# Kernel tuning notes

Hardware: AMD Instinct MI355X
Metric: run time of the kernel (lower is better)

The kernel has to match this reference:

```python
import jax, jax.numpy as jnp
import numpy as np

N_HEAD = 16
ROPE_BASE = 10000.0


def setup_inputs() -> dict:
    key = jax.random.key(0)
    k1, k2, k3 = jax.random.split(key, 3)
    B, T, C = 2, 2048, 2048
    x = jax.random.normal(k1, (B, T, C), dtype=jnp.float32)
    # 0.02 init scale keeps attention logits in a sane range
    w_qkv = jax.random.normal(k2, (3 * C, C), dtype=jnp.float32) * 0.02
    w_proj = jax.random.normal(k3, (C, C), dtype=jnp.float32) * 0.02
    return {"x": x, "w_qkv": w_qkv, "w_proj": w_proj}


def _apply_rope(t, cos, sin):
    # t: [B, T, H, hd]; cos/sin: [T, hd//2]
    B, T, H, hd = t.shape
    ts = t.reshape(B, T, H, hd // 2, 2)
    x0, x1 = ts[..., 0], ts[..., 1]
    c = cos[None, :, None, :]
    s = sin[None, :, None, :]
    out = jnp.stack([x0 * c - x1 * s, x1 * c + x0 * s], axis=-1)
    return out.reshape(B, T, H, hd)


def reference(x, w_qkv, w_proj):
    B, T, C = x.shape
    H = N_HEAD
    hd = C // H

    qkv = x @ w_qkv.T                       # [B, T, 3C]
    q, k, v = jnp.split(qkv, 3, axis=2)
    q = q.reshape(B, T, H, hd)
    k = k.reshape(B, T, H, hd)              # present kv: pre-RoPE k, [B,T,H,hd]
    v = v.reshape(B, T, H, hd).transpose(0, 2, 1, 3)  # [B,H,T,hd]

    # RoPE cache (positions = arange(T) since past_key_value is None)
    theta = 1.0 / (ROPE_BASE ** (jnp.arange(0, hd, 2, dtype=jnp.float32) / hd))
    ang = jnp.arange(T, dtype=jnp.float32)[:, None] * theta[None, :]  # [T, hd//2]
    cos, sin = jnp.cos(ang), jnp.sin(ang)

    qr = _apply_rope(q, cos, sin).transpose(0, 2, 1, 3)  # [B,H,T,hd]
    kr = _apply_rope(k, cos, sin).transpose(0, 2, 1, 3)  # [B,H,T,hd]

    scale = 1.0 / jnp.sqrt(jnp.asarray(hd, dtype=qr.dtype))
    scores = jnp.einsum('bhqd,bhkd->bhqk', qr, kr) * scale  # [B,H,T,T]
    attn = jax.nn.softmax(scores, axis=-1)
    o = jnp.einsum('bhqk,bhkd->bhqd', attn, v)              # [B,H,T,hd]
    y = o.transpose(0, 2, 1, 3).reshape(B, T, C) @ w_proj.T
    return (y, k, v)
```

## Files before the change

### kernel.cpp

```cpp
#include <hip/hip_runtime.h>
#include <math.h>


typedef __bf16 bf16_t;
typedef __bf16 bf16x8 __attribute__((ext_vector_type(8)));
typedef __bf16 bf16x4v __attribute__((ext_vector_type(4)));
typedef float  f32x4  __attribute__((ext_vector_type(4)));

#define B_  2
#define T_  2048
#define C_  2048
#define SLICE_ ((size_t)B_ * T_ * C_)

__device__ __forceinline__ void glds16(const void* g, void* l) {
  __builtin_amdgcn_global_load_lds(
      (__attribute__((address_space(1))) void*)(void*)(const_cast<void*>(g)),
      (__attribute__((address_space(3))) void*)(l), 16, 0, 0);
}

__global__ __launch_bounds__(256) void k_cvt(const float4* __restrict__ in,
                                             bf16x4v* __restrict__ out, int n4) {
  int i = blockIdx.x * 256 + threadIdx.x;
  if (i < n4) {
    float4 v = in[i];
    bf16x4v o;
    o[0] = (bf16_t)v.x; o[1] = (bf16_t)v.y; o[2] = (bf16_t)v.z; o[3] = (bf16_t)v.w;
    out[i] = o;
  }
}

__global__ __launch_bounds__(256) void k_tab(float2* __restrict__ tab) {
  int i = blockIdx.x * 256 + threadIdx.x;
  int t = i >> 6, j = i & 63;
  float thf = (float)pow(10000.0, -(double)(2 * j) / 128.0);
  float angf = (float)t * thf;
  double a = (double)angf;
  tab[i] = make_float2((float)cos(a), (float)sin(a));
}

__global__ __launch_bounds__(256, 2) void k_qkv(
    const bf16_t* __restrict__ X, const bf16_t* __restrict__ W,
    const float2* __restrict__ tab,
    bf16_t* __restrict__ qb, bf16_t* __restrict__ kb, bf16_t* __restrict__ vtb,
    float* __restrict__ kout, float* __restrict__ vout) {
  const int K = 2048;
  __shared__ alignas(16) bf16_t smem[17408];
  bf16_t* As = smem;
  bf16_t* Bs = smem + 8192;
  const int tid = threadIdx.x;
  const int lane = tid & 63, wv = tid >> 6;
  const int wm = wv >> 1, wn = wv & 1;
  const int q4 = lane >> 4, l16 = lane & 15;
  const int m0 = blockIdx.x * 128, n0 = blockIdx.y * 128;

  const bf16_t* Ab = X + (size_t)m0 * K;
  const bf16_t* Wb = W + (size_t)n0 * K;

  f32x4 zero4 = {0.f, 0.f, 0.f, 0.f};
  f32x4 acc[4][4];
#pragma unroll
  for (int i = 0; i < 4; ++i)
#pragma unroll
    for (int j = 0; j < 4; ++j) acc[i][j] = zero4;

  for (int k0 = 0; k0 < K; k0 += 64) {
    __syncthreads();
#pragma unroll
    for (int i = 0; i < 4; ++i) {
      int ci = i * 256 + tid;
      glds16(Ab + (size_t)(ci >> 3) * K + k0 + (((ci & 7) ^ ((ci >> 3) & 7)) << 3),
             &As[(i * 256 + wv * 64) * 8]);
    }
#pragma unroll
    for (int i = 0; i < 4; ++i) {
      int ci = i * 256 + tid;
      glds16(Wb + (size_t)(ci >> 3) * K + k0 + (((ci & 7) ^ ((ci >> 3) & 7)) << 3),
             &Bs[(i * 256 + wv * 64) * 8]);
    }
    __syncthreads();
#pragma unroll
    for (int kk = 0; kk < 2; ++kk) {
      bf16x8 afrag[4], bfrag[4];
#pragma unroll
      for (int mf = 0; mf < 4; ++mf)
        afrag[mf] = *(const bf16x8*)&As[(wm * 64 + mf * 16 + l16) * 64 +
                                        ((((kk << 2) | q4) ^ (l16 & 7)) << 3)];
#pragma unroll
      for (int nf = 0; nf < 4; ++nf)
        bfrag[nf] = *(const bf16x8*)&Bs[(wn * 64 + nf * 16 + l16) * 64 +
                                        ((((kk << 2) | q4) ^ (l16 & 7)) << 3)];
#pragma unroll
      for (int mf = 0; mf < 4; ++mf)
#pragma unroll
        for (int nf = 0; nf < 4; ++nf)
          acc[mf][nf] = __builtin_amdgcn_mfma_f32_16x16x32_bf16(
              afrag[mf], bfrag[nf], acc[mf][nf], 0, 0, 0);
    }
  }

  __syncthreads();
  const int sec = n0 >> 11;
  const int t0 = m0 & 2047, bb = m0 >> 11, h = (n0 & 2047) >> 7;

  if (sec < 2) {
#pragma unroll
    for (int mf = 0; mf < 4; ++mf)
#pragma unroll
      for (int nf = 0; nf < 4; ++nf)
#pragma unroll
        for (int r = 0; r < 4; ++r) {
          int ml = wm * 64 + mf * 16 + q4 * 4 + r;
          int d = wn * 64 + nf * 16 + l16;
          float val = acc[mf][nf][r];
          float partner = __shfl_xor(val, 1);
          float2 cs = tab[(t0 + ml) * 64 + (d >> 1)];
          float rv = (d & 1) ? (val * cs.x + partner * cs.y)
                             : (val * cs.x - partner * cs.y);
          if (sec == 0) rv *= 0.08838834764831845f;
          else kout[(size_t)(m0 + ml) * 2048 + h * 128 + d] = val;
          smem[ml * 136 + d] = (bf16_t)rv;
        }
    __syncthreads();
    bf16_t* dst = (sec == 0 ? qb : kb);
    size_t gbase = ((size_t)(bb * 16 + h) * 2048 + t0) * 128;
#pragma unroll
    for (int i = 0; i < 8; ++i) {
      int ci = i * 256 + tid, ml = ci >> 4, cc = (ci & 15) * 8;
      *(bf16x8*)(dst + gbase + (size_t)ml * 128 + cc) =
          *(const bf16x8*)&smem[ml * 136 + cc];
    }
  } else {
#pragma unroll
    for (int mf = 0; mf < 4; ++mf)
#pragma unroll
      for (int nf = 0; nf < 4; ++nf)
#pragma unroll
        for (int r = 0; r < 4; ++r) {
          int ml = wm * 64 + mf * 16 + q4 * 4 + r;
          int d = wn * 64 + nf * 16 + l16;
          float val = acc[mf][nf][r];
          vout[((size_t)(bb * 16 + h) * 2048 + t0 + ml) * 128 + d] = val;
          smem[d * 136 + ml] = (bf16_t)val;
        }
    __syncthreads();
#pragma unroll
    for (int i = 0; i < 8; ++i) {
      int ci = i * 256 + tid, dr = ci >> 4, cc = (ci & 15) * 8;
      *(bf16x8*)(vtb + ((size_t)((bb * 16 + h) * 128 + dr)) * 2048 + t0 + cc) =
          *(const bf16x8*)&smem[dr * 136 + cc];
    }
  }
}

__global__ __launch_bounds__(256, 2) void k_attn(
    const bf16_t* __restrict__ qb, const bf16_t* __restrict__ kb,
    const bf16_t* __restrict__ vtb, bf16_t* __restrict__ ob) {
  __shared__ alignas(16) bf16_t Ps[128 * 80];
  __shared__ alignas(16) bf16_t Ks[64 * 128];
  __shared__ alignas(16) bf16_t Vts[128 * 64];

  const int tid = threadIdx.x;
  const int lane = tid & 63, wv = tid >> 6;
  const int q4 = lane >> 4, l16 = lane & 15;
  const int bh = blockIdx.x >> 4;
  const int q0 = (blockIdx.x & 15) * 128;

  const bf16_t* Qg = qb + (size_t)bh * T_ * 128 + (size_t)q0 * 128;
  const bf16_t* Kg = kb + (size_t)bh * T_ * 128;
  const bf16_t* Vg = vtb + (size_t)bh * 128 * T_;

  bf16x8 qa[2][4];
#pragma unroll
  for (int mf = 0; mf < 2; ++mf)
#pragma unroll
    for (int kf = 0; kf < 4; ++kf)
      qa[mf][kf] = *(const bf16x8*)(Qg + (size_t)(wv * 32 + mf * 16 + l16) * 128 +
                                    kf * 32 + q4 * 8);

  f32x4 zero4 = {0.f, 0.f, 0.f, 0.f};
  float lrow[2][4];
  f32x4 oacc[2][8];
#pragma unroll
  for (int mf = 0; mf < 2; ++mf) {
#pragma unroll
    for (int r = 0; r < 4; ++r) lrow[mf][r] = 0.f;
#pragma unroll
    for (int nf = 0; nf < 8; ++nf) oacc[mf][nf] = zero4;
  }

  for (int key0 = 0; key0 < T_; key0 += 64) {
    __syncthreads();
#pragma unroll
    for (int i = 0; i < 4; ++i) {
      int ci = i * 256 + tid;
      glds16(Kg + (size_t)(key0 + (ci >> 4)) * 128 +
                 (((ci & 15) ^ ((ci >> 4) & 7)) << 3),
             &Ks[(i * 256 + wv * 64) * 8]);
    }
#pragma unroll
    for (int i = 0; i < 4; ++i) {
      int ci = i * 256 + tid;
      glds16(Vg + (size_t)(ci >> 3) * T_ + key0 +
                 (((ci & 7) ^ ((ci >> 3) & 7)) << 3),
             &Vts[(i * 256 + wv * 64) * 8]);
    }
    __syncthreads();

    f32x4 sacc[2][4];
#pragma unroll
    for (int mf = 0; mf < 2; ++mf)
#pragma unroll
      for (int nf = 0; nf < 4; ++nf) sacc[mf][nf] = zero4;
#pragma unroll
    for (int kf = 0; kf < 4; ++kf) {
      bf16x8 bfrag[4];
#pragma unroll
      for (int nf = 0; nf < 4; ++nf)
        bfrag[nf] = *(const bf16x8*)&Ks[(nf * 16 + l16) * 128 +
                                        ((((kf << 2) | q4) ^ (l16 & 7)) << 3)];
#pragma unroll
      for (int mf = 0; mf < 2; ++mf)
#pragma unroll
        for (int nf = 0; nf < 4; ++nf)
          sacc[mf][nf] = __builtin_amdgcn_mfma_f32_16x16x32_bf16(
              qa[mf][kf], bfrag[nf], sacc[mf][nf], 0, 0, 0);
    }

#pragma unroll
    for (int mf = 0; mf < 2; ++mf) {
#pragma unroll
      for (int r = 0; r < 4; ++r) {
        float p0 = __expf(sacc[mf][0][r]);
        float p1 = __expf(sacc[mf][1][r]);
        float p2 = __expf(sacc[mf][2][r]);
        float p3 = __expf(sacc[mf][3][r]);
        int prow = wv * 32 + mf * 16 + q4 * 4 + r;
        Ps[prow * 80 + 0 + l16]  = (bf16_t)p0;
        Ps[prow * 80 + 16 + l16] = (bf16_t)p1;
        Ps[prow * 80 + 32 + l16] = (bf16_t)p2;
        Ps[prow * 80 + 48 + l16] = (bf16_t)p3;
        lrow[mf][r] += (p0 + p1) + (p2 + p3);
      }
    }

#pragma unroll
    for (int kf2 = 0; kf2 < 2; ++kf2) {
      bf16x8 pa[2], vb[8];
#pragma unroll
      for (int mf = 0; mf < 2; ++mf)
        pa[mf] = *(const bf16x8*)&Ps[(wv * 32 + mf * 16 + l16) * 80 +
                                     kf2 * 32 + q4 * 8];
#pragma unroll
      for (int nf = 0; nf < 8; ++nf)
        vb[nf] = *(const bf16x8*)&Vts[(nf * 16 + l16) * 64 +
                                      ((((kf2 << 2) | q4) ^ (l16 & 7)) << 3)];
#pragma unroll
      for (int mf = 0; mf < 2; ++mf)
#pragma unroll
        for (int nf = 0; nf < 8; ++nf)
          oacc[mf][nf] = __builtin_amdgcn_mfma_f32_16x16x32_bf16(
              pa[mf], vb[nf], oacc[mf][nf], 0, 0, 0);
    }
  }

  const int b = bh >> 4, h = bh & 15;
#pragma unroll
  for (int mf = 0; mf < 2; ++mf) {
#pragma unroll
    for (int r = 0; r < 4; ++r) {
      float l = lrow[mf][r];
      l += __shfl_xor(l, 1);
      l += __shfl_xor(l, 2);
      l += __shfl_xor(l, 4);
      l += __shfl_xor(l, 8);
      float inv = 1.f / l;
      int t = q0 + wv * 32 + mf * 16 + q4 * 4 + r;
      size_t base = ((size_t)b * 2048 + t) * 2048 + h * 128;
#pragma unroll
      for (int nf = 0; nf < 8; ++nf)
        ob[base + nf * 16 + l16] = (bf16_t)(oacc[mf][nf][r] * inv);
    }
  }
}

__global__ __launch_bounds__(256, 2) void k_proj(
    const bf16_t* __restrict__ O, const bf16_t* __restrict__ Wp,
    float* __restrict__ Y) {
  const int K = 2048;
  __shared__ alignas(16) bf16_t As[128 * 64];
  __shared__ alignas(16) bf16_t Bs[128 * 64];
  const int tid = threadIdx.x;
  const int lane = tid & 63, wv = tid >> 6;
  const int wm = wv >> 1, wn = wv & 1;
  const int q4 = lane >> 4, l16 = lane & 15;
  const int m0 = blockIdx.x * 128, n0 = blockIdx.y * 128;

  const bf16_t* Ab = O + (size_t)m0 * K;
  const bf16_t* Wb = Wp + (size_t)n0 * K;

  f32x4 zero4 = {0.f, 0.f, 0.f, 0.f};
  f32x4 acc[4][4];
#pragma unroll
  for (int i = 0; i < 4; ++i)
#pragma unroll
    for (int j = 0; j < 4; ++j) acc[i][j] = zero4;

  for (int k0 = 0; k0 < K; k0 += 64) {
    __syncthreads();
#pragma unroll
    for (int i = 0; i < 4; ++i) {
      int ci = i * 256 + tid;
      glds16(Ab + (size_t)(ci >> 3) * K + k0 + (((ci & 7) ^ ((ci >> 3) & 7)) << 3),
             &As[(i * 256 + wv * 64) * 8]);
    }
#pragma unroll
    for (int i = 0; i < 4; ++i) {
      int ci = i * 256 + tid;
      glds16(Wb + (size_t)(ci >> 3) * K + k0 + (((ci & 7) ^ ((ci >> 3) & 7)) << 3),
             &Bs[(i * 256 + wv * 64) * 8]);
    }
    __syncthreads();
#pragma unroll
    for (int kk = 0; kk < 2; ++kk) {
      bf16x8 afrag[4], bfrag[4];
#pragma unroll
      for (int mf = 0; mf < 4; ++mf)
        afrag[mf] = *(const bf16x8*)&As[(wm * 64 + mf * 16 + l16) * 64 +
                                        ((((kk << 2) | q4) ^ (l16 & 7)) << 3)];
#pragma unroll
      for (int nf = 0; nf < 4; ++nf)
        bfrag[nf] = *(const bf16x8*)&Bs[(wn * 64 + nf * 16 + l16) * 64 +
                                        ((((kk << 2) | q4) ^ (l16 & 7)) << 3)];
#pragma unroll
      for (int mf = 0; mf < 4; ++mf)
#pragma unroll
        for (int nf = 0; nf < 4; ++nf)
          acc[mf][nf] = __builtin_amdgcn_mfma_f32_16x16x32_bf16(
              afrag[mf], bfrag[nf], acc[mf][nf], 0, 0, 0);
    }
  }
#pragma unroll
  for (int mf = 0; mf < 4; ++mf)
#pragma unroll
    for (int nf = 0; nf < 4; ++nf)
#pragma unroll
      for (int r = 0; r < 4; ++r) {
        int m = m0 + wm * 64 + mf * 16 + q4 * 4 + r;
        int n = n0 + wn * 64 + nf * 16 + l16;
        Y[(size_t)m * 2048 + n] = acc[mf][nf][r];
      }
}

extern "C" void kernel_launch(void* const* d_in, const int* in_sizes, int n_in,
                              void* d_out, int out_size, void* d_ws, size_t ws_size,
                              hipStream_t stream) {
  const float* x = (const float*)d_in[0];
  const float* wqkv = (const float*)d_in[1];
  const float* wproj = (const float*)d_in[2];

  float* y = (float*)d_out;
  float* kout = y + SLICE_;
  float* vout = y + 2 * SLICE_;

  char* w = (char*)d_ws;
  bf16_t* xb = (bf16_t*)w;      w += SLICE_ * 2;
  bf16_t* wqkvb = (bf16_t*)w;   w += (size_t)12582912 * 2;
  bf16_t* wprojb = (bf16_t*)w;  w += (size_t)4194304 * 2;
  bf16_t* qb = (bf16_t*)w;      w += SLICE_ * 2;
  bf16_t* kb = (bf16_t*)w;      w += SLICE_ * 2;
  bf16_t* vtb = (bf16_t*)w;     w += SLICE_ * 2;
  bf16_t* ob = (bf16_t*)w;      w += SLICE_ * 2;
  float2* tab = (float2*)w;     w += (size_t)131072 * 8;
  (void)ws_size; (void)in_sizes; (void)n_in; (void)out_size;

  k_cvt<<<8192, 256, 0, stream>>>((const float4*)x, (bf16x4v*)xb, 2097152);
  k_cvt<<<12288, 256, 0, stream>>>((const float4*)wqkv, (bf16x4v*)wqkvb, 3145728);
  k_cvt<<<4096, 256, 0, stream>>>((const float4*)wproj, (bf16x4v*)wprojb, 1048576);
  k_tab<<<512, 256, 0, stream>>>(tab);

  dim3 gq(32, 48);
  k_qkv<<<gq, 256, 0, stream>>>(xb, wqkvb, tab, qb, kb, vtb, kout, vout);
  k_attn<<<512, 256, 0, stream>>>(qb, kb, vtb, ob);
  dim3 gp(32, 16);
  k_proj<<<gp, 256, 0, stream>>>(ob, wprojb, y);
}
```

Before: 414.0 us.

## Read K/V fragments straight from global in attention and fuse conversion kernels

The attention kernel stops staging K and V^T tiles in shared memory and instead loads MFMA B-fragments directly from global memory, which removes two block barriers per key tile. Block indexing now puts batch-head in the low bits, so blocks running concurrently share K/V through L2. The three fp32-to-bf16 conversion launches become one launch that relies on xb, wqkvb and wprojb sitting contiguously in the workspace. The cost is that every wave issues its own redundant global/L2 loads of K and V with less coalesced access in place of shared-memory reuse.

```diff
diff --git a/kernel.cpp b/kernel.cpp
--- a/kernel.cpp
+++ b/kernel.cpp
@@ -18,15 +18,17 @@
       (__attribute__((address_space(3))) void*)(l), 16, 0, 0);
 }
 
-__global__ __launch_bounds__(256) void k_cvt(const float4* __restrict__ in,
-                                             bf16x4v* __restrict__ out, int n4) {
+__global__ __launch_bounds__(256) void k_cvt_all(
+    const float4* __restrict__ x, const float4* __restrict__ wq,
+    const float4* __restrict__ wp, bf16x4v* __restrict__ out) {
   int i = blockIdx.x * 256 + threadIdx.x;
-  if (i < n4) {
-    float4 v = in[i];
-    bf16x4v o;
-    o[0] = (bf16_t)v.x; o[1] = (bf16_t)v.y; o[2] = (bf16_t)v.z; o[3] = (bf16_t)v.w;
-    out[i] = o;
-  }
+  float4 v;
+  if (i < 2097152) v = x[i];
+  else if (i < 5242880) v = wq[i - 2097152];
+  else v = wp[i - 5242880];
+  bf16x4v o;
+  o[0] = (bf16_t)v.x; o[1] = (bf16_t)v.y; o[2] = (bf16_t)v.z; o[3] = (bf16_t)v.w;
+  out[i] = o;
 }
 
 __global__ __launch_bounds__(256) void k_tab(float2* __restrict__ tab) {
@@ -156,14 +158,12 @@
     const bf16_t* __restrict__ qb, const bf16_t* __restrict__ kb,
     const bf16_t* __restrict__ vtb, bf16_t* __restrict__ ob) {
   __shared__ alignas(16) bf16_t Ps[128 * 80];
-  __shared__ alignas(16) bf16_t Ks[64 * 128];
-  __shared__ alignas(16) bf16_t Vts[128 * 64];
 
   const int tid = threadIdx.x;
   const int lane = tid & 63, wv = tid >> 6;
   const int q4 = lane >> 4, l16 = lane & 15;
-  const int bh = blockIdx.x >> 4;
-  const int q0 = (blockIdx.x & 15) * 128;
+  const int bh = blockIdx.x & 31;
+  const int q0 = (blockIdx.x >> 5) * 128;
 
   const bf16_t* Qg = qb + (size_t)bh * T_ * 128 + (size_t)q0 * 128;
   const bf16_t* Kg = kb + (size_t)bh * T_ * 128;
@@ -189,23 +189,6 @@
   }
 
   for (int key0 = 0; key0 < T_; key0 += 64) {
-    __syncthreads();
-#pragma unroll
-    for (int i = 0; i < 4; ++i) {
-      int ci = i * 256 + tid;
-      glds16(Kg + (size_t)(key0 + (ci >> 4)) * 128 +
-                 (((ci & 15) ^ ((ci >> 4) & 7)) << 3),
-             &Ks[(i * 256 + wv * 64) * 8]);
-    }
-#pragma unroll
-    for (int i = 0; i < 4; ++i) {
-      int ci = i * 256 + tid;
-      glds16(Vg + (size_t)(ci >> 3) * T_ + key0 +
-                 (((ci & 7) ^ ((ci >> 3) & 7)) << 3),
-             &Vts[(i * 256 + wv * 64) * 8]);
-    }
-    __syncthreads();
-
     f32x4 sacc[2][4];
 #pragma unroll
     for (int mf = 0; mf < 2; ++mf)
@@ -216,8 +199,8 @@
       bf16x8 bfrag[4];
 #pragma unroll
       for (int nf = 0; nf < 4; ++nf)
-        bfrag[nf] = *(const bf16x8*)&Ks[(nf * 16 + l16) * 128 +
-                                        ((((kf << 2) | q4) ^ (l16 & 7)) << 3)];
+        bfrag[nf] = *(const bf16x8*)(Kg + (size_t)(key0 + nf * 16 + l16) * 128 +
+                                     kf * 32 + q4 * 8);
 #pragma unroll
       for (int mf = 0; mf < 2; ++mf)
 #pragma unroll
@@ -252,8 +235,8 @@
                                      kf2 * 32 + q4 * 8];
 #pragma unroll
       for (int nf = 0; nf < 8; ++nf)
-        vb[nf] = *(const bf16x8*)&Vts[(nf * 16 + l16) * 64 +
-                                      ((((kf2 << 2) | q4) ^ (l16 & 7)) << 3)];
+        vb[nf] = *(const bf16x8*)(Vg + (size_t)(nf * 16 + l16) * 2048 + key0 +
+                                  kf2 * 32 + q4 * 8);
 #pragma unroll
       for (int mf = 0; mf < 2; ++mf)
 #pragma unroll
@@ -373,9 +356,8 @@
   float2* tab = (float2*)w;     w += (size_t)131072 * 8;
   (void)ws_size; (void)in_sizes; (void)n_in; (void)out_size;
 
-  k_cvt<<<8192, 256, 0, stream>>>((const float4*)x, (bf16x4v*)xb, 2097152);
-  k_cvt<<<12288, 256, 0, stream>>>((const float4*)wqkv, (bf16x4v*)wqkvb, 3145728);
-  k_cvt<<<4096, 256, 0, stream>>>((const float4*)wproj, (bf16x4v*)wprojb, 1048576);
+  k_cvt_all<<<24576, 256, 0, stream>>>((const float4*)x, (const float4*)wqkv,
+                                       (const float4*)wproj, (bf16x4v*)xb);
   k_tab<<<512, 256, 0, stream>>>(tab);
 
   dim3 gq(32, 48);
```

Result: slower. 551.5 us (+33.2%).
